# Optimization experiments

Measured on AMD Instinct MI355X. Metric: run time of the kernel, lower is better.

Reference implementation:

```python
import jax, jax.numpy as jnp
import numpy as np
from jax import lax

N = 16384
K = 16
EPS = 1e-5


def setup_inputs() -> dict:
    key = jax.random.key(0)
    ks = jax.random.split(key, 10)

    def w(k, shape):
        fan_in = shape[0]
        return jax.random.normal(k, shape, jnp.float32) / np.sqrt(fan_in)

    return {
        "pos": jax.random.normal(ks[0], (N, 3), jnp.float32),
        "normal": jax.random.normal(ks[1], (N, 3), jnp.float32),
        # conv1 mlp: Linear(9,64) -> GroupNorm(8,64) -> ReLU -> Linear(64,64)
        "W1a": w(ks[2], (9, 64)), "b1a": jnp.zeros((64,), jnp.float32),
        "g1": jnp.ones((64,), jnp.float32), "beta1": jnp.zeros((64,), jnp.float32),
        "W1b": w(ks[3], (64, 64)), "b1b": jnp.zeros((64,), jnp.float32),
        # conv2 mlp: Linear(67,64) -> GroupNorm(8,64) -> ReLU -> Linear(64,64)
        "W2a": w(ks[4], (67, 64)), "b2a": jnp.zeros((64,), jnp.float32),
        "g2": jnp.ones((64,), jnp.float32), "beta2": jnp.zeros((64,), jnp.float32),
        "W2b": w(ks[5], (64, 64)), "b2b": jnp.zeros((64,), jnp.float32),
        # conv3 mlp: Linear(67,128) -> GroupNorm(16,128) -> ReLU -> Linear(128,128)
        "W3a": w(ks[6], (67, 128)), "b3a": jnp.zeros((128,), jnp.float32),
        "g3": jnp.ones((128,), jnp.float32), "beta3": jnp.zeros((128,), jnp.float32),
        "W3b": w(ks[7], (128, 128)), "b3b": jnp.zeros((128,), jnp.float32),
    }


def knn_graph(pos, k):
    # [N,N] squared distances; loop=True -> self is included (distance 0).
    sq = jnp.sum(pos * pos, axis=1)
    d2 = sq[:, None] + sq[None, :] - 2.0 * (pos @ pos.T)
    _, nbr = lax.top_k(-d2, k)  # [N,k] neighbor (source) indices per target node
    return nbr


def group_norm(h, gamma, beta, groups):
    # h: [N,k,C]; normalize each group of channels per edge sample.
    n, k, c = h.shape
    hg = h.reshape(n, k, groups, c // groups)
    mu = hg.mean(axis=-1, keepdims=True)
    var = hg.var(axis=-1, keepdims=True)
    hg = (hg - mu) * lax.rsqrt(var + EPS)
    return hg.reshape(n, k, c) * gamma + beta


def pointnet_conv(x, pos, nbr, Wa, ba, gamma, beta, Wb, bb, groups):
    # message: concat(x_j, pos_j - pos_i), MLP per edge, max-aggregate over neighbors
    xj = x[nbr]                              # [N,k,C_in]
    rel = pos[nbr] - pos[:, None, :]         # [N,k,3]
    m = jnp.concatenate([xj, rel], axis=-1)  # [N,k,C_in+3]
    h = m @ Wa + ba
    h = jax.nn.relu(group_norm(h, gamma, beta, groups))
    h = h @ Wb + bb
    return jnp.max(h, axis=1)                # [N,C_out]


def reference(pos, normal, W1a, b1a, g1, beta1, W1b, b1b,
              W2a, b2a, g2, beta2, W2b, b2b,
              W3a, b3a, g3, beta3, W3b, b3b):
    nbr = knn_graph(pos, K)
    h = jnp.concatenate([pos, normal], axis=-1)  # [N,6]
    h1 = jax.nn.relu(pointnet_conv(h, pos, nbr, W1a, b1a, g1, beta1, W1b, b1b, 8))
    h2 = jax.nn.relu(pointnet_conv(h1, pos, nbr, W2a, b2a, g2, beta2, W2b, b2b, 8))
    h3 = jax.nn.relu(pointnet_conv(h2, pos, nbr, W3a, b3a, g3, beta3, W3b, b3b, 16))
    return (h1, h2, h3)
```

## Files before the change

kernel.cpp:

```cpp
#include <hip/hip_runtime.h>
#include <hip/hip_bf16.h>
#include <stdint.h>

typedef unsigned long long u64;
typedef unsigned int u32;
typedef __attribute__((ext_vector_type(8))) short bf16x8;
typedef __attribute__((ext_vector_type(8))) unsigned short u16x8;
typedef __attribute__((ext_vector_type(4))) float f32x4;

__device__ __forceinline__ float ldv(const void* p, size_t idx, int mode) {
  return mode ? __bfloat162float(((const __hip_bfloat16*)p)[idx])
              : ((const float*)p)[idx];
}
__device__ __forceinline__ void stv(void* p, size_t idx, int mode, float v) {
  if (mode) ((__hip_bfloat16*)p)[idx] = __float2bfloat16(v);
  else      ((float*)p)[idx] = v;
}
__device__ __forceinline__ unsigned short f2bfb(float f) {
  u32 u = __float_as_uint(f);
  u32 r = u + 0x7fffu + ((u >> 16) & 1u);
  return (unsigned short)(r >> 16);
}
__device__ __forceinline__ float bfb2f(unsigned short b) {
  return __uint_as_float((u32)b << 16);
}
__device__ __forceinline__ u64 shfl64(u64 v, int src) {
  int lo = __shfl((int)(u32)(v & 0xffffffffu), src, 64);
  int hi = __shfl((int)(u32)(v >> 32), src, 64);
  return ((u64)(u32)hi << 32) | (u32)lo;
}
__device__ __forceinline__ u64 shflxor64(u64 v, int m) {
  int lo = __shfl_xor((int)(u32)(v & 0xffffffffu), m, 64);
  int hi = __shfl_xor((int)(u32)(v >> 32), m, 64);
  return ((u64)(u32)hi << 32) | (u32)lo;
}
__device__ __forceinline__ u64 shfl64w16(u64 v, int src) {
  int lo = __shfl((int)(u32)(v & 0xffffffffu), src, 16);
  int hi = __shfl((int)(u32)(v >> 32), src, 16);
  return ((u64)(u32)hi << 32) | (u32)lo;
}

__global__ void PointNetSimple_61409442398998_kernel() {}

struct CvtEnt { const void* src; float* dst; int n; };
struct CvtArgs { CvtEnt e[12]; };
struct WEnt { const void* src; unsigned short* dst; int K, N, Kpad; };
struct WArgs { WEnt e[6]; };

__global__ void setup_kernel(const void* __restrict__ pos,
                             const void* __restrict__ nrm,
                             WArgs wa, CvtArgs ca,
                             int* __restrict__ flag,
                             float4* __restrict__ pos4,
                             float* __restrict__ h0, int n) {
  const unsigned short* u16p = (const unsigned short*)pos;
  int cnt = 0;
  for (int k = 0; k < 32; ++k) {
    int e = (u16p[k] >> 7) & 0xff;
    if (e >= 110 && e <= 140) cnt++;
  }
  const int mode = (cnt >= 26) ? 1 : 0;

  const int nprep = n >> 8;
  const int b = blockIdx.x;
  if (b < nprep) {
    int i = b * 256 + threadIdx.x;
    float x = ldv(pos, 3*(size_t)i+0, mode);
    float y = ldv(pos, 3*(size_t)i+1, mode);
    float z = ldv(pos, 3*(size_t)i+2, mode);
    pos4[i] = make_float4(x, y, z, x*x + y*y + z*z);
    h0[6*(size_t)i+0] = x; h0[6*(size_t)i+1] = y; h0[6*(size_t)i+2] = z;
    h0[6*(size_t)i+3] = ldv(nrm, 3*(size_t)i+0, mode);
    h0[6*(size_t)i+4] = ldv(nrm, 3*(size_t)i+1, mode);
    h0[6*(size_t)i+5] = ldv(nrm, 3*(size_t)i+2, mode);
  } else {
    int r = b - nprep;
    if (r < 6) {
      WEnt ent = wa.e[r];
      for (int t = threadIdx.x; t < ent.N * ent.Kpad; t += blockDim.x) {
        int nn = t / ent.Kpad;
        int k  = t - nn * ent.Kpad;
        float v = (k < ent.K) ? ldv(ent.src, (size_t)k * ent.N + nn, mode) : 0.0f;
        ent.dst[t] = f2bfb(v);
      }
      if (r == 0 && threadIdx.x == 0) flag[0] = mode;
    } else {
      for (int t2 = 0; t2 < 12; ++t2) {
        CvtEnt ent = ca.e[t2];
        for (int t = threadIdx.x; t < ent.n; t += blockDim.x)
          ent.dst[t] = ldv(ent.src, t, mode);
      }
    }
  }
}

#define KNN_TPB 512
#define KNN_WPB 8
#define KCH 1024

__device__ __forceinline__ void knn_flush(u64* __restrict__ wbuf, int& cnt,
                                          u64& val, u64& t15, float& th,
                                          int lane) {
  u64 cand = (lane < cnt) ? wbuf[lane] : ~0ull;
#pragma unroll
  for (int k = 2; k <= 64; k <<= 1) {
#pragma unroll
    for (int j = k >> 1; j > 0; j >>= 1) {
      u64 other = shflxor64(cand, j);
      bool up    = ((lane & k) == 0) || (k == 64);
      bool lower = ((lane & j) == 0);
      bool keepMin = (up == lower);
      u64 mn = cand < other ? cand : other;
      u64 mx = cand < other ? other : cand;
      cand = keepMin ? mn : mx;
    }
  }
  u64 rev = shfl64w16(cand, 15 - (lane & 15));
  u64 lo = val < rev ? val : rev;
#pragma unroll
  for (int j = 8; j > 0; j >>= 1) {
    u64 other = shflxor64(lo, j);
    bool lower = ((lane & j) == 0);
    u64 mn = lo < other ? lo : other;
    u64 mx = lo < other ? other : lo;
    lo = lower ? mn : mx;
  }
  val = (lane < 16) ? lo : ~0ull;
  t15 = shfl64(val, 15);
  th = __uint_as_float((u32)(t15 >> 32));
  cnt = 0;
}

__global__ __launch_bounds__(KNN_TPB) void knn4_kernel(
    const float4* __restrict__ pos4, int* __restrict__ nbr, int n) {
  __shared__ float4 sp[2][KCH];
  __shared__ u64 buf[KNN_WPB][72];
  const int tid  = threadIdx.x;
  const int lane = tid & 63;
  const int wid  = tid >> 6;
  const int i    = blockIdx.x * KNN_WPB + wid;
  const float4 pi = pos4[i];
  u64* wbuf = &buf[wid][0];

  u64 val = ~0ull;
  u64 t15 = ~0ull;
  float th = 3.4e38f;
  int cnt = 0;

  for (int t = tid; t < KCH; t += KNN_TPB) sp[0][t] = pos4[t];
  __syncthreads();

  const int nch = n / KCH;
  for (int c = 0; c < nch; ++c) {
    const int cur = c & 1;
    float4 pre0, pre1;
    const bool more = (c + 1 < nch);
    if (more) {
      pre0 = pos4[(size_t)(c+1)*KCH + tid];
      pre1 = pos4[(size_t)(c+1)*KCH + KNN_TPB + tid];
    }
#pragma unroll 2
    for (int t = 0; t < KCH; t += 64) {
      float4 a = sp[cur][t + lane];
      float d2 = (pi.w + a.w) - 2.0f*(pi.x*a.x + pi.y*a.y + pi.z*a.z);
      d2 = fmaxf(d2, 0.0f);
      bool pass = (d2 <= th);
      u64 bal = __ballot(pass);
      if (bal) {
        int pc = __popcll(bal);
        if (cnt + pc > 64) knn_flush(wbuf, cnt, val, t15, th, lane);
        u32 mb = __builtin_amdgcn_mbcnt_lo((u32)bal, 0u);
        mb = __builtin_amdgcn_mbcnt_hi((u32)(bal >> 32), mb);
        if (pass)
          wbuf[cnt + mb] = ((u64)__float_as_uint(d2) << 32) | (u32)(c*KCH + t + lane);
        cnt += pc;
      }
    }
    if (more) {
      sp[cur^1][tid] = pre0;
      sp[cur^1][KNN_TPB + tid] = pre1;
    }
    __syncthreads();
  }
  knn_flush(wbuf, cnt, val, t15, th, lane);
  if (lane < 16) nbr[(size_t)i*16 + lane] = (int)(val & 0xffffffffu);
}

template<int CIN, int CMID, int KT1, int NT, int KT2>
__global__ __launch_bounds__(256, 4) void conv_mfma6_kernel(
    const float* __restrict__ xf,
    const unsigned short* __restrict__ xb,
    const float4* __restrict__ pos4,
    const int* __restrict__ nbr,
    const int* __restrict__ flag,
    const unsigned short* __restrict__ WaT,
    const unsigned short* __restrict__ WbT,
    const float* __restrict__ baf,
    const float* __restrict__ gmf,
    const float* __restrict__ btf,
    const float* __restrict__ bbf,
    unsigned short* __restrict__ xoutb,
    void* __restrict__ bout, size_t out_off)
{
  constexpr int K1PAD = KT1 * 32;
  constexpr int SB = CMID + 8;

  __shared__ unsigned short msgB[128 * SB];

  const int tid  = threadIdx.x;
  const int lane = tid & 63;
  const int w    = tid >> 6;
  const int quad = lane >> 4;
  const int cl   = lane & 15;
  const int node0 = blockIdx.x * 8;
  const int mode = flag[0];

  bf16x8 afr[2][KT1];
#pragma unroll
  for (int mt = 0; mt < 2; ++mt) {
    const int node = node0 + w*2 + mt;
    const int j = nbr[(size_t)node*16 + cl];
    const float4 pin = pos4[node];
    const float4 pj = pos4[j];
    const float rx = pj.x - pin.x, ry = pj.y - pin.y, rz = pj.z - pin.z;
    if constexpr (CIN == 64) {
#pragma unroll
      for (int kt = 0; kt < 2; ++kt)
        afr[mt][kt] = *(const bf16x8*)&xb[(size_t)j*64 + kt*32 + quad*8];
      unsigned short o[8] = {0,0,0,0,0,0,0,0};
      if (quad == 0) { o[0] = f2bfb(rx); o[1] = f2bfb(ry); o[2] = f2bfb(rz); }
      afr[mt][KT1-1] = *(bf16x8*)o;
    } else {
      unsigned short o[8] = {0,0,0,0,0,0,0,0};
      if (quad == 0) {
        const float* p = &xf[(size_t)j*6];
        o[0] = f2bfb(p[0]); o[1] = f2bfb(p[1]); o[2] = f2bfb(p[2]);
        o[3] = f2bfb(p[3]); o[4] = f2bfb(p[4]); o[5] = f2bfb(p[5]);
        o[6] = f2bfb(rx);   o[7] = f2bfb(ry);
      } else if (quad == 1) {
        o[0] = f2bfb(rz);
      }
      afr[mt][0] = *(bf16x8*)o;
    }
  }

  const int grow = lane >> 1, ggl = lane & 1;
#pragma unroll
  for (int nt = 0; nt < NT; ++nt) {
    f32x4 a1[2];
    a1[0] = (f32x4){0.f, 0.f, 0.f, 0.f};
    a1[1] = (f32x4){0.f, 0.f, 0.f, 0.f};
#pragma unroll
    for (int kt = 0; kt < KT1; ++kt) {
      bf16x8 bfr = *(const bf16x8*)&WaT[(size_t)(nt*16 + cl) * K1PAD + kt*32 + quad*8];
      a1[0] = __builtin_amdgcn_mfma_f32_16x16x32_bf16(afr[0][kt], bfr, a1[0], 0, 0, 0);
      a1[1] = __builtin_amdgcn_mfma_f32_16x16x32_bf16(afr[1][kt], bfr, a1[1], 0, 0, 0);
    }
    float bac = baf[nt*16 + cl];
#pragma unroll
    for (int mt = 0; mt < 2; ++mt)
#pragma unroll
      for (int reg = 0; reg < 4; ++reg)
        msgB[(w*32 + mt*16 + quad*4 + reg) * SB + nt*16 + cl] =
            f2bfb(a1[mt][reg] + bac);
    asm volatile("" ::: "memory");
    {
      const int cb = nt*16 + ggl*8;
      unsigned short* p = &msgB[(w*32 + grow) * SB + cb];
      u16x8 hv = *(const u16x8*)p;
      float vv[8];
#pragma unroll
      for (int e = 0; e < 8; ++e) vv[e] = bfb2f(hv[e]);
      float s = 0.f, q = 0.f;
#pragma unroll
      for (int e = 0; e < 8; ++e) { s += vv[e]; q += vv[e]*vv[e]; }
      float mu = s * 0.125f;
      float var = q * 0.125f - mu * mu;
      float inv = rsqrtf(fmaxf(var, 0.0f) + 1e-5f);
      unsigned short o[8];
#pragma unroll
      for (int e = 0; e < 8; ++e) {
        float t = (vv[e] - mu) * inv * gmf[cb+e] + btf[cb+e];
        o[e] = f2bfb(fmaxf(t, 0.0f));
      }
      *(bf16x8*)p = *(bf16x8*)o;
    }
    asm volatile("" ::: "memory");
  }

  f32x4 acc2[2][NT];
#pragma unroll
  for (int mt = 0; mt < 2; ++mt)
#pragma unroll
    for (int nt = 0; nt < NT; ++nt) acc2[mt][nt] = (f32x4){0.f, 0.f, 0.f, 0.f};
#pragma unroll
  for (int kt = 0; kt < KT2; ++kt) {
    bf16x8 af0 = *(const bf16x8*)&msgB[(w*32 + cl)      * SB + kt*32 + quad*8];
    bf16x8 af1 = *(const bf16x8*)&msgB[(w*32 + 16 + cl) * SB + kt*32 + quad*8];
#pragma unroll
    for (int nt = 0; nt < NT; ++nt) {
      bf16x8 bfr = *(const bf16x8*)&WbT[(size_t)(nt*16 + cl) * CMID + kt*32 + quad*8];
      acc2[0][nt] = __builtin_amdgcn_mfma_f32_16x16x32_bf16(af0, bfr, acc2[0][nt], 0, 0, 0);
      acc2[1][nt] = __builtin_amdgcn_mfma_f32_16x16x32_bf16(af1, bfr, acc2[1][nt], 0, 0, 0);
    }
  }

#pragma unroll
  for (int mt = 0; mt < 2; ++mt) {
    int node = node0 + w*2 + mt;
#pragma unroll
    for (int nt = 0; nt < NT; ++nt) {
      float m = fmaxf(fmaxf(acc2[mt][nt][0], acc2[mt][nt][1]),
                      fmaxf(acc2[mt][nt][2], acc2[mt][nt][3]));
      m = fmaxf(m, __shfl_xor(m, 16, 64));
      m = fmaxf(m, __shfl_xor(m, 32, 64));
      float v = fmaxf(m + bbf[nt*16 + cl], 0.0f);
      if (quad == 0) {
        size_t oi = (size_t)node * CMID + nt*16 + cl;
        if (xoutb) xoutb[oi] = f2bfb(v);
        stv(bout, out_off + oi, mode, v);
      }
    }
  }
}

extern "C" void kernel_launch(void* const* d_in, const int* in_sizes, int n_in,
                              void* d_out, int out_size, void* d_ws, size_t ws_size,
                              hipStream_t stream) {
  (void)n_in; (void)ws_size; (void)in_sizes;
  int n = out_size / 256;
  if (n <= 0 || (n & 255)) n = 16384;

  float* ws = (float*)d_ws;
  int*    flag    = (int*)ws;
  float4* pos4    = (float4*)(ws + 16);
  float*  h0      = ws + 16 + (size_t)4*n;
  int*    nbr     = (int*)(ws + 16 + (size_t)10*n);
  unsigned short* h1b = (unsigned short*)(ws + 16 + (size_t)26*n);
  unsigned short* h2b = (unsigned short*)(ws + 16 + (size_t)58*n);
  float*  vbuf    = ws + 16 + (size_t)90*n;
  unsigned short* wtbuf = (unsigned short*)(vbuf + 1024);

  const int vsz[12] = {64,64,64,64, 64,64,64,64, 128,128,128,128};
  const int vsrc[12] = {3,4,5,7, 9,10,11,13, 15,16,17,19};
  CvtArgs ca;
  float* vptr[12];
  {
    int off = 0;
    for (int t = 0; t < 12; ++t) {
      ca.e[t].src = d_in[vsrc[t]];
      ca.e[t].dst = vbuf + off;
      ca.e[t].n   = vsz[t];
      vptr[t] = vbuf + off;
      off += vsz[t];
    }
  }
  const int wK[6]    = {9, 64, 67, 64, 67, 128};
  const int wN[6]    = {64, 64, 64, 64, 128, 128};
  const int wKp[6]   = {32, 64, 96, 64, 96, 128};
  const int wsrc[6]  = {2, 6, 8, 12, 14, 18};
  WArgs wa;
  unsigned short* wptr[6];
  {
    int off = 0;
    for (int t = 0; t < 6; ++t) {
      wa.e[t].src  = d_in[wsrc[t]];
      wa.e[t].dst  = wtbuf + off;
      wa.e[t].K    = wK[t];
      wa.e[t].N    = wN[t];
      wa.e[t].Kpad = wKp[t];
      wptr[t] = wtbuf + off;
      off += wN[t] * wKp[t];
    }
  }

  setup_kernel<<<n/256 + 7, 256, 0, stream>>>(
      d_in[0], d_in[1], wa, ca, flag, pos4, h0, n);
  knn4_kernel<<<n/KNN_WPB, KNN_TPB, 0, stream>>>(pos4, nbr, n);

  conv_mfma6_kernel<6, 64, 1, 4, 2><<<n/8, 256, 0, stream>>>(
      h0, (const unsigned short*)nullptr, pos4, nbr, flag, wptr[0], wptr[1],
      vptr[0], vptr[1], vptr[2], vptr[3], h1b, d_out, (size_t)0);
  conv_mfma6_kernel<64, 64, 3, 4, 2><<<n/8, 256, 0, stream>>>(
      (const float*)nullptr, h1b, pos4, nbr, flag, wptr[2], wptr[3],
      vptr[4], vptr[5], vptr[6], vptr[7], h2b, d_out, (size_t)n*64);
  conv_mfma6_kernel<64, 128, 3, 8, 4><<<n/8, 256, 0, stream>>>(
      (const float*)nullptr, h2b, pos4, nbr, flag, wptr[4], wptr[5],
      vptr[8], vptr[9], vptr[10], vptr[11],
      (unsigned short*)nullptr, d_out, (size_t)n*128);
}
```

Before: 373.4 us.

## Replace brute-force kNN with uniform-grid spatial search

Swaps the O(N^2) brute-force kNN scan for a 32^3 uniform grid. Points are bounded, binned, prefix-summed and scattered into cell order, then each query searches expanding shells of cells until the distance to the shell boundary exceeds the current 16th-nearest threshold. This cuts distance evaluations from N per query to a local neighbourhood. In exchange it adds several small launches, atomics, and a single-block scan. Tie ordering among equal distances may differ from the brute-force version because candidates arrive in cell order.

```diff
diff --git a/kernel.cpp b/kernel.cpp
--- a/kernel.cpp
+++ b/kernel.cpp
@@ -38,6 +38,15 @@
   int lo = __shfl((int)(u32)(v & 0xffffffffu), src, 16);
   int hi = __shfl((int)(u32)(v >> 32), src, 16);
   return ((u64)(u32)hi << 32) | (u32)lo;
+}
+
+__device__ __forceinline__ u32 benc(float f) {
+  u32 u = __float_as_uint(f);
+  return (u & 0x80000000u) ? ~u : (u | 0x80000000u);
+}
+__device__ __forceinline__ float bdec(u32 k) {
+  return (k & 0x80000000u) ? __uint_as_float(k ^ 0x80000000u)
+                           : __uint_as_float(~k);
 }
 
 __global__ void PointNetSimple_61409442398998_kernel() {}
@@ -83,7 +92,12 @@
         float v = (k < ent.K) ? ldv(ent.src, (size_t)k * ent.N + nn, mode) : 0.0f;
         ent.dst[t] = f2bfb(v);
       }
-      if (r == 0 && threadIdx.x == 0) flag[0] = mode;
+      if (r == 0 && threadIdx.x == 0) {
+        flag[0] = mode;
+        u32* bb = (u32*)flag;
+        bb[4] = bb[5] = bb[6] = 0xffffffffu;
+        bb[7] = bb[8] = bb[9] = 0u;
+      }
     } else {
       for (int t2 = 0; t2 < 12; ++t2) {
         CvtEnt ent = ca.e[t2];
@@ -93,10 +107,6 @@
     }
   }
 }
-
-#define KNN_TPB 512
-#define KNN_WPB 8
-#define KCH 1024
 
 __device__ __forceinline__ void knn_flush(u64* __restrict__ wbuf, int& cnt,
                                           u64& val, u64& t15, float& th,
@@ -127,44 +137,136 @@
   }
   val = (lane < 16) ? lo : ~0ull;
   t15 = shfl64(val, 15);
-  th = __uint_as_float((u32)(t15 >> 32));
+  u32 thb = (u32)(t15 >> 32);
+  th = (thb == 0xffffffffu) ? 3.4e38f : __uint_as_float(thb);
   cnt = 0;
 }
 
-__global__ __launch_bounds__(KNN_TPB) void knn4_kernel(
-    const float4* __restrict__ pos4, int* __restrict__ nbr, int n) {
-  __shared__ float4 sp[2][KCH];
-  __shared__ u64 buf[KNN_WPB][72];
-  const int tid  = threadIdx.x;
-  const int lane = tid & 63;
-  const int wid  = tid >> 6;
-  const int i    = blockIdx.x * KNN_WPB + wid;
+#define GR 32
+#define GR3 (GR*GR*GR)
+
+__global__ __launch_bounds__(256) void grid0_kernel(
+    const float4* __restrict__ pos4, int* __restrict__ counts,
+    u32* __restrict__ bbx, int n) {
+  const int t = blockIdx.x * 256 + threadIdx.x;
+  const int stride = gridDim.x * 256;
+  for (int idx = t; idx < GR3; idx += stride) counts[idx] = 0;
+  float mn[3] = {3.4e38f, 3.4e38f, 3.4e38f};
+  float mx[3] = {-3.4e38f, -3.4e38f, -3.4e38f};
+  for (int i = t; i < n; i += stride) {
+    float4 p = pos4[i];
+    mn[0] = fminf(mn[0], p.x); mx[0] = fmaxf(mx[0], p.x);
+    mn[1] = fminf(mn[1], p.y); mx[1] = fmaxf(mx[1], p.y);
+    mn[2] = fminf(mn[2], p.z); mx[2] = fmaxf(mx[2], p.z);
+  }
+#pragma unroll
+  for (int m = 32; m; m >>= 1) {
+#pragma unroll
+    for (int k = 0; k < 3; ++k) {
+      mn[k] = fminf(mn[k], __shfl_xor(mn[k], m, 64));
+      mx[k] = fmaxf(mx[k], __shfl_xor(mx[k], m, 64));
+    }
+  }
+  if ((threadIdx.x & 63) == 0) {
+#pragma unroll
+    for (int k = 0; k < 3; ++k) {
+      atomicMin(&bbx[k],     benc(mn[k]));
+      atomicMax(&bbx[3 + k], benc(mx[k]));
+    }
+  }
+}
+
+__global__ __launch_bounds__(256) void hist_kernel(
+    const float4* __restrict__ pos4, const u32* __restrict__ bbx,
+    int* __restrict__ counts, int* __restrict__ cid, int n) {
+  const int i = blockIdx.x * 256 + threadIdx.x;
+  if (i >= n) return;
+  const float mnx = bdec(bbx[0]), mny = bdec(bbx[1]), mnz = bdec(bbx[2]);
+  const float ihx = (float)GR / fmaxf(bdec(bbx[3]) - mnx, 1e-20f);
+  const float ihy = (float)GR / fmaxf(bdec(bbx[4]) - mny, 1e-20f);
+  const float ihz = (float)GR / fmaxf(bdec(bbx[5]) - mnz, 1e-20f);
+  float4 p = pos4[i];
+  int cx = min(GR - 1, max(0, (int)((p.x - mnx) * ihx)));
+  int cy = min(GR - 1, max(0, (int)((p.y - mny) * ihy)));
+  int cz = min(GR - 1, max(0, (int)((p.z - mnz) * ihz)));
+  int lin = (cz * GR + cy) * GR + cx;
+  cid[i] = lin;
+  atomicAdd(&counts[lin], 1);
+}
+
+__global__ __launch_bounds__(1024) void scan_kernel(
+    const int* __restrict__ counts, int* __restrict__ cellstart,
+    int* __restrict__ cursor) {
+  __shared__ int part[1024];
+  const int t = threadIdx.x;
+  const int base = t * 32;
+  int v[32];
+  int s = 0;
+#pragma unroll
+  for (int k = 0; k < 32; ++k) { v[k] = counts[base + k]; s += v[k]; }
+  part[t] = s;
+  __syncthreads();
+  for (int d = 1; d < 1024; d <<= 1) {
+    int x = (t >= d) ? part[t - d] : 0;
+    __syncthreads();
+    part[t] += x;
+    __syncthreads();
+  }
+  int off = part[t] - s;
+#pragma unroll
+  for (int k = 0; k < 32; ++k) {
+    cellstart[base + k] = off; cursor[base + k] = off; off += v[k];
+  }
+  if (t == 1023) { cellstart[GR3] = off; cursor[GR3] = off; }
+}
+
+__global__ __launch_bounds__(256) void scatter_kernel(
+    const float4* __restrict__ pos4, const int* __restrict__ cid,
+    int* __restrict__ cursor, int* __restrict__ sidx,
+    float4* __restrict__ spos4, int n) {
+  const int i = blockIdx.x * 256 + threadIdx.x;
+  if (i >= n) return;
+  int dst = atomicAdd(&cursor[cid[i]], 1);
+  spos4[dst] = pos4[i];
+  sidx[dst]  = i;
+}
+
+#define KNN5_WPB 4
+__global__ __launch_bounds__(256) void knn5_kernel(
+    const float4* __restrict__ pos4, const float4* __restrict__ spos4,
+    const int* __restrict__ sidx, const int* __restrict__ cellstart,
+    const u32* __restrict__ bbx, int* __restrict__ nbr, int n) {
+  __shared__ u64 buf[KNN5_WPB][72];
+  const int tid = threadIdx.x, lane = tid & 63, w = tid >> 6;
+  const int i = blockIdx.x * KNN5_WPB + w;
+  u64* wbuf = &buf[w][0];
   const float4 pi = pos4[i];
-  u64* wbuf = &buf[wid][0];
-
-  u64 val = ~0ull;
-  u64 t15 = ~0ull;
+
+  const float mnx = bdec(bbx[0]), mny = bdec(bbx[1]), mnz = bdec(bbx[2]);
+  const float ex = fmaxf(bdec(bbx[3]) - mnx, 1e-20f);
+  const float ey = fmaxf(bdec(bbx[4]) - mny, 1e-20f);
+  const float ez = fmaxf(bdec(bbx[5]) - mnz, 1e-20f);
+  const float ihx = (float)GR / ex, ihy = (float)GR / ey, ihz = (float)GR / ez;
+  const float hxf = ex * (1.0f / GR), hyf = ey * (1.0f / GR), hzf = ez * (1.0f / GR);
+  const int cx = min(GR - 1, max(0, (int)((pi.x - mnx) * ihx)));
+  const int cy = min(GR - 1, max(0, (int)((pi.y - mny) * ihy)));
+  const int cz = min(GR - 1, max(0, (int)((pi.z - mnz) * ihz)));
+
+  u64 val = ~0ull, t15 = ~0ull;
   float th = 3.4e38f;
-  int cnt = 0;
-
-  for (int t = tid; t < KCH; t += KNN_TPB) sp[0][t] = pos4[t];
-  __syncthreads();
-
-  const int nch = n / KCH;
-  for (int c = 0; c < nch; ++c) {
-    const int cur = c & 1;
-    float4 pre0, pre1;
-    const bool more = (c + 1 < nch);
-    if (more) {
-      pre0 = pos4[(size_t)(c+1)*KCH + tid];
-      pre1 = pos4[(size_t)(c+1)*KCH + KNN_TPB + tid];
-    }
-#pragma unroll 2
-    for (int t = 0; t < KCH; t += 64) {
-      float4 a = sp[cur][t + lane];
+  int cnt = 0, nseen = 0;
+
+  auto procRange = [&](int c0, int c1) {
+    int p0 = cellstart[c0];
+    int p1 = cellstart[c1 + 1];
+    nseen += p1 - p0;
+    for (int t0 = p0; t0 < p1; t0 += 64) {
+      int g = t0 + lane;
+      bool in = g < p1;
+      float4 a = spos4[in ? g : (p1 - 1)];
       float d2 = (pi.w + a.w) - 2.0f*(pi.x*a.x + pi.y*a.y + pi.z*a.z);
       d2 = fmaxf(d2, 0.0f);
-      bool pass = (d2 <= th);
+      bool pass = in && (d2 <= th);
       u64 bal = __ballot(pass);
       if (bal) {
         int pc = __popcll(bal);
@@ -172,18 +274,43 @@
         u32 mb = __builtin_amdgcn_mbcnt_lo((u32)bal, 0u);
         mb = __builtin_amdgcn_mbcnt_hi((u32)(bal >> 32), mb);
         if (pass)
-          wbuf[cnt + mb] = ((u64)__float_as_uint(d2) << 32) | (u32)(c*KCH + t + lane);
+          wbuf[cnt + mb] = ((u64)__float_as_uint(d2) << 32) | (u32)sidx[g];
         cnt += pc;
       }
     }
-    if (more) {
-      sp[cur^1][tid] = pre0;
-      sp[cur^1][KNN_TPB + tid] = pre1;
-    }
-    __syncthreads();
-  }
-  knn_flush(wbuf, cnt, val, t15, th, lane);
-  if (lane < 16) nbr[(size_t)i*16 + lane] = (int)(val & 0xffffffffu);
+  };
+
+  for (int r = 0; r < GR; ++r) {
+    for (int dz = -r; dz <= r; ++dz) {
+      int z = cz + dz;
+      if ((unsigned)z >= GR) continue;
+      for (int dy = -r; dy <= r; ++dy) {
+        int y = cy + dy;
+        if ((unsigned)y >= GR) continue;
+        int rowbase = (z * GR + y) * GR;
+        if (dz == -r || dz == r || dy == -r || dy == r) {
+          int lo = max(cx - r, 0), hi = min(cx + r, GR - 1);
+          procRange(rowbase + lo, rowbase + hi);
+        } else {
+          if (cx - r >= 0) procRange(rowbase + cx - r, rowbase + cx - r);
+          if (cx + r < GR) procRange(rowbase + cx + r, rowbase + cx + r);
+        }
+      }
+    }
+    if (cnt > 0) knn_flush(wbuf, cnt, val, t15, th, lane);
+    if (nseen >= n) break;
+    float mind = 3.4e38f;
+    if (cx - r > 0)      mind = fminf(mind, pi.x - (mnx + (float)(cx - r) * hxf));
+    if (cx + r < GR - 1) mind = fminf(mind, (mnx + (float)(cx + r + 1) * hxf) - pi.x);
+    if (cy - r > 0)      mind = fminf(mind, pi.y - (mny + (float)(cy - r) * hyf));
+    if (cy + r < GR - 1) mind = fminf(mind, (mny + (float)(cy + r + 1) * hyf) - pi.y);
+    if (cz - r > 0)      mind = fminf(mind, pi.z - (mnz + (float)(cz - r) * hzf));
+    if (cz + r < GR - 1) mind = fminf(mind, (mnz + (float)(cz + r + 1) * hzf) - pi.z);
+    float mind2 = mind * mind * 0.9999f - 1e-6f;
+    if (mind2 > th) break;
+  }
+  if (cnt > 0) knn_flush(wbuf, cnt, val, t15, th, lane);
+  if (lane < 16) nbr[(size_t)i * 16 + lane] = (int)(val & 0xffffffffu);
 }
 
 template<int CIN, int CMID, int KT1, int NT, int KT2>
@@ -341,6 +468,14 @@
   float*  vbuf    = ws + 16 + (size_t)90*n;
   unsigned short* wtbuf = (unsigned short*)(vbuf + 1024);
 
+  float* gbase = vbuf + 1024 + 22528;
+  int*    cid       = (int*)gbase;
+  int*    counts    = cid + n;
+  int*    cellstart = counts + GR3;
+  int*    cursor    = cellstart + 32772;
+  int*    sidx      = cursor + 32772;
+  float4* spos4     = (float4*)(sidx + n);
+
   const int vsz[12] = {64,64,64,64, 64,64,64,64, 128,128,128,128};
   const int vsrc[12] = {3,4,5,7, 9,10,11,13, 15,16,17,19};
   CvtArgs ca;
@@ -376,7 +511,14 @@
 
   setup_kernel<<<n/256 + 7, 256, 0, stream>>>(
       d_in[0], d_in[1], wa, ca, flag, pos4, h0, n);
-  knn4_kernel<<<n/KNN_WPB, KNN_TPB, 0, stream>>>(pos4, nbr, n);
+
+  u32* bbx = (u32*)ws + 4;
+  grid0_kernel<<<256, 256, 0, stream>>>(pos4, counts, bbx, n);
+  hist_kernel<<<n/256, 256, 0, stream>>>(pos4, bbx, counts, cid, n);
+  scan_kernel<<<1, 1024, 0, stream>>>(counts, cellstart, cursor);
+  scatter_kernel<<<n/256, 256, 0, stream>>>(pos4, cid, cursor, sidx, spos4, n);
+  knn5_kernel<<<n/KNN5_WPB, 256, 0, stream>>>(pos4, spos4, sidx, cellstart,
+                                              bbx, nbr, n);
 
   conv_mfma6_kernel<6, 64, 1, 4, 2><<<n/8, 256, 0, stream>>>(
       h0, (const unsigned short*)nullptr, pos4, nbr, flag, wptr[0], wptr[1],
```

Measured after the change: 609.2 us. 1.63x slower.
